# Kernel tuning notes

Hardware: AMD Instinct MI355X
Metric: run time of the kernel (lower is better)

## Reference

```python
import jax, jax.numpy as jnp
import numpy as np

EPS = 1e-6  # flax.linen.LayerNorm default

def layer_norm(x, scale, bias):
    mean = jnp.mean(x, axis=-1, keepdims=True)
    var = jnp.mean(jnp.square(x - mean), axis=-1, keepdims=True)
    return (x - mean) * jax.lax.rsqrt(var + EPS) * scale + bias

def setup_inputs() -> dict:
    key = jax.random.key(0)
    ks = jax.random.split(key, 4)
    B, P, D, H = 2, 2048, 768, 12
    hd = D // H
    x = jax.random.normal(ks[0], (B, P, D), dtype=jnp.float32)
    W_qkv = jax.random.normal(ks[1], (D, 3 * D), dtype=jnp.float32) * (D ** -0.5)
    W_out = jax.random.normal(ks[2], (D, D), dtype=jnp.float32) * (D ** -0.5)
    b_out = jnp.zeros((D,), dtype=jnp.float32)
    return {
        "x": x,
        "W_qkv": W_qkv,
        "q_scale": jnp.ones((hd,), jnp.float32),
        "q_bias": jnp.zeros((hd,), jnp.float32),
        "k_scale": jnp.ones((hd,), jnp.float32),
        "k_bias": jnp.zeros((hd,), jnp.float32),
        "o_scale": jnp.ones((D,), jnp.float32),
        "o_bias": jnp.zeros((D,), jnp.float32),
        "W_out": W_out,
        "b_out": b_out,
    }

def reference(x, W_qkv, q_scale, q_bias, k_scale, k_bias, o_scale, o_bias, W_out, b_out):
    B, P, D = x.shape
    H = 12
    hd = D // H
    scale = hd ** -0.5
    # fused QKV projection, no bias
    qkv = (x @ W_qkv).reshape(B, P, 3, H, hd).transpose(2, 0, 3, 1, 4)  # [3,B,H,P,hd]
    q, k, v = qkv[0], qkv[1], qkv[2]
    # per-head QK LayerNorm over head_dim
    q = layer_norm(q, q_scale, q_bias) * scale
    k = layer_norm(k, k_scale, k_bias)
    attn = jnp.einsum("bhqd,bhkd->bhqk", q, k)
    attn = jax.nn.softmax(attn, axis=-1)
    out = jnp.einsum("bhqk,bhkd->bhqd", attn, v)  # [B,H,P,hd]
    out = jnp.swapaxes(out, 1, 2).reshape(B, P, D)
    out = layer_norm(out, o_scale, o_bias)
    return out @ W_out + b_out
```

## Files before the change

### kernel.cpp

```cpp
#include <hip/hip_runtime.h>
#include <hip/hip_bf16.h>

#define B_  2
#define P_  2048
#define D_  768
#define H_  12
#define HD_ 64
#define M_  (B_ * P_)
#define N1_ (3 * D_)

typedef __attribute__((ext_vector_type(8))) short short8;
typedef __attribute__((ext_vector_type(4))) float f32x4;
typedef __attribute__((ext_vector_type(16))) float f32x16;
typedef __attribute__((ext_vector_type(4))) unsigned u32x4;
typedef unsigned short ushort;

__device__ __forceinline__ ushort f2bf(float f) {
    unsigned u = __float_as_uint(f);
    u += 0x7fffu + ((u >> 16) & 1u);
    return (ushort)(u >> 16);
}

__device__ __forceinline__ unsigned cvtpk(float a, float b) {
    unsigned r;
    asm("v_cvt_pk_bf16_f32 %0, %1, %2" : "=v"(r) : "v"(a), "v"(b));
    return r;
}

__device__ __forceinline__ float bf2f(ushort u) {
    return __uint_as_float((unsigned)u << 16);
}

__device__ __forceinline__ int swap23(int s) {
    return (s & ~12) | ((s & 4) << 1) | ((s & 8) >> 1);
}

#define QSC_ (0.125f * 1.44269504088896340736f)

__global__ __launch_bounds__(512) void gemm_qkv_mfma(
        const float* __restrict__ x, const float* __restrict__ w,
        const float* __restrict__ qs, const float* __restrict__ qb,
        const float* __restrict__ ks, const float* __restrict__ kb,
        ushort* __restrict__ qkv) {
    __shared__ __align__(16) ushort As[2][128][40];
    __shared__ __align__(16) ushort Bs[2][128][40];

    const int tid  = threadIdx.x;
    const int lane = tid & 63;
    const int wv   = tid >> 6;
    const int quad = lane >> 4;
    const int col  = lane & 15;
    const int wr   = (wv >> 1) * 32;
    const int wc   = (wv & 1) * 64;
    const int rowBase = blockIdx.y * 128;
    const int colBase = blockIdx.x * 128;

    const int am0 = tid >> 3, ac4 = tid & 7;
    const int nB  = tid & 127, kq = tid >> 7;

    float4 apre[2];
    float  bpre[8];
    auto load_tile = [&](int kt) {
        const int k0 = kt * 32;
        apre[0] = *(const float4*)(x + (size_t)(rowBase + am0) * D_ + k0 + ac4 * 4);
        apre[1] = *(const float4*)(x + (size_t)(rowBase + am0 + 64) * D_ + k0 + ac4 * 4);
#pragma unroll
        for (int j = 0; j < 8; j++)
            bpre[j] = w[(size_t)(k0 + kq * 8 + j) * N1_ + colBase + nB];
    };
    auto stage = [&](int buf) {
        uint2 a0 = {cvtpk(apre[0].x, apre[0].y), cvtpk(apre[0].z, apre[0].w)};
        uint2 a1 = {cvtpk(apre[1].x, apre[1].y), cvtpk(apre[1].z, apre[1].w)};
        *(uint2*)&As[buf][am0][ac4 * 4]      = a0;
        *(uint2*)&As[buf][am0 + 64][ac4 * 4] = a1;
        u32x4 bb;
#pragma unroll
        for (int j = 0; j < 4; j++) bb[j] = cvtpk(bpre[2 * j], bpre[2 * j + 1]);
        *(u32x4*)&Bs[buf][nB][kq * 8] = bb;
    };

    f32x4 acc[2][4];
#pragma unroll
    for (int i = 0; i < 2; i++)
#pragma unroll
        for (int j = 0; j < 4; j++) acc[i][j] = (f32x4){0.f, 0.f, 0.f, 0.f};

    load_tile(0);
    stage(0);
    __syncthreads();

    const int NT = D_ / 32;
    int cur = 0;
    for (int kt = 0; kt < NT; kt++) {
        const bool more = (kt + 1 < NT);
        if (more) load_tile(kt + 1);

        short8 af[2], bf[4];
#pragma unroll
        for (int mt = 0; mt < 2; mt++) af[mt] = *(const short8*)&As[cur][wr + mt * 16 + col][quad * 8];
#pragma unroll
        for (int nt = 0; nt < 4; nt++) bf[nt] = *(const short8*)&Bs[cur][wc + nt * 16 + col][quad * 8];
#pragma unroll
        for (int mt = 0; mt < 2; mt++)
#pragma unroll
            for (int nt = 0; nt < 4; nt++)
                acc[mt][nt] = __builtin_amdgcn_mfma_f32_16x16x32_bf16(af[mt], bf[nt], acc[mt][nt], 0, 0, 0);

        if (more) {
            stage(cur ^ 1);
            __syncthreads();
            cur ^= 1;
        }
    }

    const int comp = colBase / D_;
    const int rem  = colBase + wc - comp * D_;
    const int h    = rem >> 6;
    float sc4[4] = {0, 0, 0, 0}, bi4[4] = {0, 0, 0, 0};
    if (comp == 0) {
#pragma unroll
        for (int nt = 0; nt < 4; nt++) { sc4[nt] = qs[nt * 16 + col]; bi4[nt] = qb[nt * 16 + col]; }
    } else if (comp == 1) {
#pragma unroll
        for (int nt = 0; nt < 4; nt++) { sc4[nt] = ks[nt * 16 + col]; bi4[nt] = kb[nt * 16 + col]; }
    }

#pragma unroll
    for (int mt = 0; mt < 2; mt++) {
#pragma unroll
        for (int r = 0; r < 4; r++) {
            int m  = rowBase + wr + mt * 16 + quad * 4 + r;
            int bb = m >> 11;
            int p  = m & 2047;
            float v0 = acc[mt][0][r], v1 = acc[mt][1][r], v2 = acc[mt][2][r], v3 = acc[mt][3][r];
            if (comp < 2) {
                float s = v0 + v1 + v2 + v3;
#pragma unroll
                for (int off = 1; off < 16; off <<= 1) s += __shfl_xor(s, off, 64);
                float mean = s * (1.0f / 64.0f);
                float d0 = v0 - mean, d1 = v1 - mean, d2 = v2 - mean, d3 = v3 - mean;
                float sq = d0 * d0 + d1 * d1 + d2 * d2 + d3 * d3;
#pragma unroll
                for (int off = 1; off < 16; off <<= 1) sq += __shfl_xor(sq, off, 64);
                float inv = rsqrtf(sq * (1.0f / 64.0f) + 1e-6f);
                v0 = d0 * inv * sc4[0] + bi4[0];
                v1 = d1 * inv * sc4[1] + bi4[1];
                v2 = d2 * inv * sc4[2] + bi4[2];
                v3 = d3 * inv * sc4[3] + bi4[3];
                if (comp == 0) { v0 *= QSC_; v1 *= QSC_; v2 *= QSC_; v3 *= QSC_; }
            }
            size_t base = ((((size_t)comp * B_ + bb) * H_ + h) * P_ + p) * HD_;
            qkv[base +  0 + col] = f2bf(v0);
            qkv[base + 16 + col] = f2bf(v1);
            qkv[base + 32 + col] = f2bf(v2);
            qkv[base + 48 + col] = f2bf(v3);
        }
    }
}

__global__ __launch_bounds__(256) void attn_split(const ushort* __restrict__ qkv,
                                                  ushort* __restrict__ o0, ushort* __restrict__ o1,
                                                  ushort* __restrict__ o2, ushort* __restrict__ o3,
                                                  float* __restrict__ l0, float* __restrict__ l1,
                                                  float* __restrict__ l2, float* __restrict__ l3) {
    const int p0  = blockIdx.x * 128;
    const int bh  = blockIdx.y;
    const int s   = blockIdx.z;
    const int nsp = gridDim.z;
    const int b   = bh / H_, h = bh % H_;
    ushort* opart = (s == 0) ? o0 : (s == 1) ? o1 : (s == 2) ? o2 : o3;
    float*  lpart = (s == 0) ? l0 : (s == 1) ? l1 : (s == 2) ? l2 : l3;
    const int tid  = threadIdx.x;
    const int lane = tid & 63;
    const int wv   = tid >> 6;
    const int half = lane >> 5;
    const int n32  = lane & 31;

    __shared__ __align__(16) ushort KVs[2][2][64][72];

    const size_t hs  = (size_t)P_ * HD_;
    const int    kv0 = s * (P_ / nsp);
    const ushort* qg = qkv + ((size_t)(0 * B_ + b) * H_ + h) * hs + (size_t)(p0 + wv * 32) * HD_;
    const ushort* kg = qkv + ((size_t)(1 * B_ + b) * H_ + h) * hs + (size_t)kv0 * HD_;
    const ushort* vg = qkv + ((size_t)(2 * B_ + b) * H_ + h) * hs + (size_t)kv0 * HD_;

    short8 aq[4];
#pragma unroll
    for (int ks2 = 0; ks2 < 4; ks2++)
        aq[ks2] = *(const short8*)(qg + (size_t)n32 * HD_ + ks2 * 16 + half * 8);

    float lsum = 0.f;
    f32x16 oaccT[2];
#pragma unroll
    for (int nt = 0; nt < 2; nt++)
#pragma unroll
        for (int r = 0; r < 16; r++) oaccT[nt][r] = 0.f;

    const int kr = tid >> 3, kc8 = tid & 7;
    const int krs = swap23(kr);
    const int vd = tid & 63,  vkh = tid >> 6;

    uint4  kpre[2];
    ushort vpre[16];
    auto load_tile = [&](int kt) {
        const ushort* kg_t = kg + (size_t)kt * 64 * HD_;
        const ushort* vg_t = vg + (size_t)kt * 64 * HD_;
        kpre[0] = *(const uint4*)(kg_t + (size_t)kr * HD_ + kc8 * 8);
        kpre[1] = *(const uint4*)(kg_t + (size_t)(kr + 32) * HD_ + kc8 * 8);
#pragma unroll
        for (int j = 0; j < 16; j++)
            vpre[j] = vg_t[(size_t)(vkh * 16 + j) * HD_ + vd];
    };
    auto stage = [&](int buf) {
        *(uint4*)&KVs[buf][0][krs][kc8 * 8]      = kpre[0];
        *(uint4*)&KVs[buf][0][krs + 32][kc8 * 8] = kpre[1];
        *(short8*)&KVs[buf][1][vd][vkh * 16]     = *(short8*)&vpre[0];
        *(short8*)&KVs[buf][1][vd][vkh * 16 + 8] = *(short8*)&vpre[8];
    };

    load_tile(0);
    stage(0);
    __syncthreads();

    const int NT = (P_ / 64) / nsp;
    int cur = 0;
    for (int kt = 0; kt < NT; kt++) {
        const bool more = (kt + 1 < NT);
        if (more) load_tile(kt + 1);

        ushort (*Ks)[72] = KVs[cur][0];
        ushort (*Vs)[72] = KVs[cur][1];

#pragma unroll
        for (int nt = 0; nt < 2; nt++) {
            f32x16 sc;
#pragma unroll
            for (int r = 0; r < 16; r++) sc[r] = 0.f;
#pragma unroll
            for (int ks2 = 0; ks2 < 4; ks2++) {
                short8 kb2 = *(const short8*)&Ks[nt * 32 + n32][ks2 * 16 + half * 8];
                sc = __builtin_amdgcn_mfma_f32_32x32x16_bf16(kb2, aq[ks2], sc, 0, 0, 0);
            }
            float p[16];
#pragma unroll
            for (int r = 0; r < 16; r++) {
                p[r] = __builtin_amdgcn_exp2f(sc[r]);
                lsum += p[r];
            }
            unsigned w[8];
#pragma unroll
            for (int i = 0; i < 8; i++) w[i] = cvtpk(p[2 * i], p[2 * i + 1]);
#pragma unroll
            for (int kp2 = 0; kp2 < 2; kp2++) {
                u32x4 t = {w[kp2 * 4 + 0], w[kp2 * 4 + 1], w[kp2 * 4 + 2], w[kp2 * 4 + 3]};
                short8 pb = __builtin_bit_cast(short8, t);
                const int kstep = nt * 2 + kp2;
#pragma unroll
                for (int ntd = 0; ntd < 2; ntd++) {
                    short8 av = *(const short8*)&Vs[ntd * 32 + n32][kstep * 16 + half * 8];
                    oaccT[ntd] = __builtin_amdgcn_mfma_f32_32x32x16_bf16(av, pb, oaccT[ntd], 0, 0, 0);
                }
            }
        }

        if (more) {
            stage(cur ^ 1);
            __syncthreads();
            cur ^= 1;
        }
    }

    lsum += __shfl_xor(lsum, 32, 64);
    if (lane < 32)
        lpart[(size_t)bh * P_ + p0 + wv * 32 + lane] = lsum;

    float* scr = (float*)&KVs[0][0][0][0] + wv * 1152;
#pragma unroll
    for (int ntd = 0; ntd < 2; ntd++) {
#pragma unroll
        for (int r = 0; r < 16; r++)
            scr[n32 * 36 + (r & 3) + 8 * (r >> 2) + 4 * half] = oaccT[ntd][r];
#pragma unroll
        for (int i = 0; i < 4; i++) {
            int ql = i * 8 + (lane >> 3);
            int c4 = lane & 7;
            float4 v = *(const float4*)&scr[ql * 36 + c4 * 4];
            uint2 pk = {cvtpk(v.x, v.y), cvtpk(v.z, v.w)};
            *(uint2*)(opart + ((size_t)bh * P_ + p0 + wv * 32 + ql) * HD_ + ntd * 32 + c4 * 4) = pk;
        }
    }
}

__global__ __launch_bounds__(256) void ln_o(const ushort* __restrict__ o0,
                                            const ushort* __restrict__ o1,
                                            const ushort* __restrict__ o2,
                                            const ushort* __restrict__ o3,
                                            const float* __restrict__ l0,
                                            const float* __restrict__ l1,
                                            const float* __restrict__ l2,
                                            const float* __restrict__ l3,
                                            const int ns,
                                            ushort* __restrict__ lnb,
                                            const float* __restrict__ osc,
                                            const float* __restrict__ ob) {
    __shared__ float red[4];
    __shared__ float red2[4];
    const int row = blockIdx.x;
    const int b   = row >> 11;
    const int p   = row & (P_ - 1);
    const int tid = threadIdx.x;

    auto src = [&](int d) {
        int h = d >> 6;
        size_t lr  = (size_t)(b * H_ + h) * P_ + p;
        size_t idx = lr * HD_ + (d & 63);
        float num = bf2f(o0[idx]) + bf2f(o1[idx]);
        float den = l0[lr] + l1[lr];
        if (ns == 4) { num += bf2f(o2[idx]) + bf2f(o3[idx]); den += l2[lr] + l3[lr]; }
        return num / den;
    };
    float v0 = src(tid);
    float v1 = src(tid + 256);
    float v2 = src(tid + 512);
    float s = v0 + v1 + v2;
#pragma unroll
    for (int o = 32; o > 0; o >>= 1) s += __shfl_xor(s, o, 64);
    if ((tid & 63) == 0) red[tid >> 6] = s;
    __syncthreads();
    float mean = (red[0] + red[1] + red[2] + red[3]) * (1.0f / 768.0f);
    float d0 = v0 - mean, d1 = v1 - mean, d2 = v2 - mean;
    float sq = d0 * d0 + d1 * d1 + d2 * d2;
#pragma unroll
    for (int o = 32; o > 0; o >>= 1) sq += __shfl_xor(sq, o, 64);
    if ((tid & 63) == 0) red2[tid >> 6] = sq;
    __syncthreads();
    float var = (red2[0] + red2[1] + red2[2] + red2[3]) * (1.0f / 768.0f);
    float inv = rsqrtf(var + 1e-6f);
    const size_t base = (size_t)row * D_;
    lnb[base + tid]       = f2bf(d0 * inv * osc[tid]       + ob[tid]);
    lnb[base + tid + 256] = f2bf(d1 * inv * osc[tid + 256] + ob[tid + 256]);
    lnb[base + tid + 512] = f2bf(d2 * inv * osc[tid + 512] + ob[tid + 512]);
}

__global__ __launch_bounds__(256) void gemm_out_mfma(
        const ushort* __restrict__ a, const float* __restrict__ w,
        const float* __restrict__ bias, float* __restrict__ out) {
    __shared__ __align__(16) ushort As[2][64][40];
    __shared__ __align__(16) ushort Bs[2][64][40];

    const int tid  = threadIdx.x;
    const int lane = tid & 63;
    const int wv   = tid >> 6;
    const int quad = lane >> 4;
    const int col  = lane & 15;
    const int wr   = (wv >> 1) * 32;
    const int wc   = (wv & 1) * 32;
    const int rowBase = blockIdx.y * 64;
    const int colBase = blockIdx.x * 64;

    const int am  = tid >> 2, ac8 = tid & 3;
    const int nB  = tid & 63, kq = tid >> 6;

    uint4 apre;
    float bpre[8];
    auto load_tile = [&](int kt) {
        const int k0 = kt * 32;
        apre = *(const uint4*)(a + (size_t)(rowBase + am) * D_ + k0 + ac8 * 8);
#pragma unroll
        for (int j = 0; j < 8; j++)
            bpre[j] = w[(size_t)(k0 + kq * 8 + j) * D_ + colBase + nB];
    };
    auto stage = [&](int buf) {
        *(uint4*)&As[buf][am][ac8 * 8] = apre;
        u32x4 bb;
#pragma unroll
        for (int j = 0; j < 4; j++) bb[j] = cvtpk(bpre[2 * j], bpre[2 * j + 1]);
        *(u32x4*)&Bs[buf][nB][kq * 8] = bb;
    };

    f32x4 acc[2][2];
#pragma unroll
    for (int i = 0; i < 2; i++)
#pragma unroll
        for (int j = 0; j < 2; j++) acc[i][j] = (f32x4){0.f, 0.f, 0.f, 0.f};

    load_tile(0);
    stage(0);
    __syncthreads();

    const int NT = D_ / 32;
    int cur = 0;
    for (int kt = 0; kt < NT; kt++) {
        const bool more = (kt + 1 < NT);
        if (more) load_tile(kt + 1);

        short8 af[2], bf[2];
#pragma unroll
        for (int mt = 0; mt < 2; mt++) af[mt] = *(const short8*)&As[cur][wr + mt * 16 + col][quad * 8];
#pragma unroll
        for (int nt = 0; nt < 2; nt++) bf[nt] = *(const short8*)&Bs[cur][wc + nt * 16 + col][quad * 8];
#pragma unroll
        for (int mt = 0; mt < 2; mt++)
#pragma unroll
            for (int nt = 0; nt < 2; nt++)
                acc[mt][nt] = __builtin_amdgcn_mfma_f32_16x16x32_bf16(af[mt], bf[nt], acc[mt][nt], 0, 0, 0);

        if (more) {
            stage(cur ^ 1);
            __syncthreads();
            cur ^= 1;
        }
    }

    float b2[2];
#pragma unroll
    for (int nt = 0; nt < 2; nt++) b2[nt] = bias[colBase + wc + nt * 16 + col];
#pragma unroll
    for (int mt = 0; mt < 2; mt++) {
#pragma unroll
        for (int r = 0; r < 4; r++) {
            int m = rowBase + wr + mt * 16 + quad * 4 + r;
            float* dst = out + (size_t)m * D_ + colBase + wc;
#pragma unroll
            for (int nt = 0; nt < 2; nt++)
                dst[nt * 16 + col] = acc[mt][nt][r] + b2[nt];
        }
    }
}

extern "C" void kernel_launch(void* const* d_in, const int* in_sizes, int n_in,
                              void* d_out, int out_size, void* d_ws, size_t ws_size,
                              hipStream_t stream) {
    const float* x    = (const float*)d_in[0];
    const float* Wqkv = (const float*)d_in[1];
    const float* qs   = (const float*)d_in[2];
    const float* qb   = (const float*)d_in[3];
    const float* ks   = (const float*)d_in[4];
    const float* kb   = (const float*)d_in[5];
    const float* osc  = (const float*)d_in[6];
    const float* ob   = (const float*)d_in[7];
    const float* Wout = (const float*)d_in[8];
    const float* bout = (const float*)d_in[9];
    float* out = (float*)d_out;

    ushort* qkv = (ushort*)d_ws;
    const size_t qkvE = (size_t)3 * B_ * H_ * P_ * HD_;
    const size_t oE   = (size_t)B_ * H_ * P_ * HD_;
    const size_t lE   = (size_t)B_ * H_ * P_;
    ushort* obase = qkv + qkvE;
    const size_t need4 = (qkvE + 3 * oE) * sizeof(ushort) + 4 * lE * sizeof(float);
    const int nsp = (ws_size >= need4) ? 4 : 2;
    ushort* op[4];
    float* lbase;
    if (nsp == 4) {
        op[0] = obase; op[1] = obase + oE; op[2] = obase + 2 * oE; op[3] = (ushort*)out;
        lbase = (float*)(obase + 3 * oE);
    } else {
        op[0] = obase; op[1] = (ushort*)out; op[2] = obase; op[3] = obase;
        lbase = (float*)(obase + oE);
    }
    float* lp[4] = {lbase, lbase + lE, lbase + 2 * lE, lbase + 3 * lE};
    ushort* ln_buf = qkv;

    gemm_qkv_mfma<<<dim3(N1_ / 128, M_ / 128), 512, 0, stream>>>(x, Wqkv, qs, qb, ks, kb, qkv);
    attn_split<<<dim3(P_ / 128, B_ * H_, nsp), 256, 0, stream>>>(
        qkv, op[0], op[1], op[2], op[3], lp[0], lp[1], lp[2], lp[3]);
    ln_o<<<dim3(M_), 256, 0, stream>>>(
        op[0], op[1], op[2], op[3], lp[0], lp[1], lp[2], lp[3], nsp, ln_buf, osc, ob);
    gemm_out_mfma<<<dim3(D_ / 64, M_ / 64), 256, 0, stream>>>(ln_buf, Wout, bout, out);
}
```

Baseline: 207.6 us.

## Load GEMM A operands straight into registers, deepen K-tile, remap blocks per XCD

Both projection GEMMs stop staging the A operand in shared memory. Each wave loads its own rows from global memory directly in MFMA fragment layout, and only the weight tile goes through LDS. The K step doubles to 64 and the tiles change: 128x64 with 256 threads for QKV, 64x64 for the output GEMM. A 1D grid with an XCD-aware swizzle groups row tiles per XCD for L2 locality. The aim is less LDS traffic and fewer barriers. The cost is uncoalesced, redundant A reads from global memory, since each wave re-reads the full A rows for its column tile.

```diff
diff --git a/kernel.cpp b/kernel.cpp
--- a/kernel.cpp
+++ b/kernel.cpp
@@ -37,46 +37,58 @@
 
 #define QSC_ (0.125f * 1.44269504088896340736f)
 
-__global__ __launch_bounds__(512) void gemm_qkv_mfma(
+__global__ __launch_bounds__(256) void gemm_qkv_mfma(
         const float* __restrict__ x, const float* __restrict__ w,
         const float* __restrict__ qs, const float* __restrict__ qb,
         const float* __restrict__ ks, const float* __restrict__ kb,
         ushort* __restrict__ qkv) {
-    __shared__ __align__(16) ushort As[2][128][40];
-    __shared__ __align__(16) ushort Bs[2][128][40];
+    __shared__ __align__(16) ushort Bs[2][64][72];
+
+    const int L   = blockIdx.x;
+    const int xcd = L & 7;
+    const int idx = L >> 3;
+    const int by  = xcd + 8 * (idx / 36);
+    const int bx  = idx % 36;
+    const int rowBase = by * 128;
+    const int colBase = bx * 64;
 
     const int tid  = threadIdx.x;
     const int lane = tid & 63;
     const int wv   = tid >> 6;
     const int quad = lane >> 4;
     const int col  = lane & 15;
-    const int wr   = (wv >> 1) * 32;
-    const int wc   = (wv & 1) * 64;
-    const int rowBase = blockIdx.y * 128;
-    const int colBase = blockIdx.x * 128;
-
-    const int am0 = tid >> 3, ac4 = tid & 7;
-    const int nB  = tid & 127, kq = tid >> 7;
-
-    float4 apre[2];
-    float  bpre[8];
-    auto load_tile = [&](int kt) {
-        const int k0 = kt * 32;
-        apre[0] = *(const float4*)(x + (size_t)(rowBase + am0) * D_ + k0 + ac4 * 4);
-        apre[1] = *(const float4*)(x + (size_t)(rowBase + am0 + 64) * D_ + k0 + ac4 * 4);
-#pragma unroll
-        for (int j = 0; j < 8; j++)
-            bpre[j] = w[(size_t)(k0 + kq * 8 + j) * N1_ + colBase + nB];
-    };
-    auto stage = [&](int buf) {
-        uint2 a0 = {cvtpk(apre[0].x, apre[0].y), cvtpk(apre[0].z, apre[0].w)};
-        uint2 a1 = {cvtpk(apre[1].x, apre[1].y), cvtpk(apre[1].z, apre[1].w)};
-        *(uint2*)&As[buf][am0][ac4 * 4]      = a0;
-        *(uint2*)&As[buf][am0 + 64][ac4 * 4] = a1;
-        u32x4 bb;
-#pragma unroll
-        for (int j = 0; j < 4; j++) bb[j] = cvtpk(bpre[2 * j], bpre[2 * j + 1]);
-        *(u32x4*)&Bs[buf][nB][kq * 8] = bb;
+
+    const int nB = tid & 63, kg = tid >> 6;
+
+    float bpre[16];
+    auto load_b = [&](int kt) {
+        const int k0 = kt * 64;
+#pragma unroll
+        for (int j = 0; j < 16; j++)
+            bpre[j] = w[(size_t)(k0 + kg * 16 + j) * N1_ + colBase + nB];
+    };
+    auto stage_b = [&](int buf) {
+        u32x4 b0, b1;
+#pragma unroll
+        for (int j = 0; j < 4; j++) b0[j] = cvtpk(bpre[2 * j], bpre[2 * j + 1]);
+#pragma unroll
+        for (int j = 0; j < 4; j++) b1[j] = cvtpk(bpre[8 + 2 * j], bpre[8 + 2 * j + 1]);
+        *(u32x4*)&Bs[buf][nB][kg * 16]     = b0;
+        *(u32x4*)&Bs[buf][nB][kg * 16 + 8] = b1;
+    };
+
+    const float* arow0 = x + (size_t)(rowBase + wv * 32 + col) * D_ + quad * 8;
+    const float* arow1 = arow0 + (size_t)16 * D_;
+    float4 apre[2][2][2];
+    auto load_a = [&](int kt) {
+        const int k0 = kt * 64;
+#pragma unroll
+        for (int k32 = 0; k32 < 2; k32++) {
+            apre[0][k32][0] = *(const float4*)(arow0 + k0 + k32 * 32);
+            apre[0][k32][1] = *(const float4*)(arow0 + k0 + k32 * 32 + 4);
+            apre[1][k32][0] = *(const float4*)(arow1 + k0 + k32 * 32);
+            apre[1][k32][1] = *(const float4*)(arow1 + k0 + k32 * 32 + 4);
+        }
     };
 
     f32x4 acc[2][4];
@@ -85,36 +97,53 @@
 #pragma unroll
         for (int j = 0; j < 4; j++) acc[i][j] = (f32x4){0.f, 0.f, 0.f, 0.f};
 
-    load_tile(0);
-    stage(0);
+    load_a(0);
+    load_b(0);
+    stage_b(0);
     __syncthreads();
 
-    const int NT = D_ / 32;
+    const int NT = D_ / 64;
     int cur = 0;
     for (int kt = 0; kt < NT; kt++) {
         const bool more = (kt + 1 < NT);
-        if (more) load_tile(kt + 1);
-
-        short8 af[2], bf[4];
-#pragma unroll
-        for (int mt = 0; mt < 2; mt++) af[mt] = *(const short8*)&As[cur][wr + mt * 16 + col][quad * 8];
-#pragma unroll
-        for (int nt = 0; nt < 4; nt++) bf[nt] = *(const short8*)&Bs[cur][wc + nt * 16 + col][quad * 8];
+
+        short8 af[2][2];
 #pragma unroll
         for (int mt = 0; mt < 2; mt++)
 #pragma unroll
+            for (int k32 = 0; k32 < 2; k32++) {
+                u32x4 t;
+                t[0] = cvtpk(apre[mt][k32][0].x, apre[mt][k32][0].y);
+                t[1] = cvtpk(apre[mt][k32][0].z, apre[mt][k32][0].w);
+                t[2] = cvtpk(apre[mt][k32][1].x, apre[mt][k32][1].y);
+                t[3] = cvtpk(apre[mt][k32][1].z, apre[mt][k32][1].w);
+                af[mt][k32] = __builtin_bit_cast(short8, t);
+            }
+
+        if (more) { load_a(kt + 1); load_b(kt + 1); }
+
+#pragma unroll
+        for (int k32 = 0; k32 < 2; k32++) {
+            short8 bf[4];
+#pragma unroll
             for (int nt = 0; nt < 4; nt++)
-                acc[mt][nt] = __builtin_amdgcn_mfma_f32_16x16x32_bf16(af[mt], bf[nt], acc[mt][nt], 0, 0, 0);
+                bf[nt] = *(const short8*)&Bs[cur][nt * 16 + col][k32 * 32 + quad * 8];
+#pragma unroll
+            for (int mt = 0; mt < 2; mt++)
+#pragma unroll
+                for (int nt = 0; nt < 4; nt++)
+                    acc[mt][nt] = __builtin_amdgcn_mfma_f32_16x16x32_bf16(af[mt][k32], bf[nt], acc[mt][nt], 0, 0, 0);
+        }
 
         if (more) {
-            stage(cur ^ 1);
+            stage_b(cur ^ 1);
             __syncthreads();
             cur ^= 1;
         }
     }
 
     const int comp = colBase / D_;
-    const int rem  = colBase + wc - comp * D_;
+    const int rem  = colBase - comp * D_;
     const int h    = rem >> 6;
     float sc4[4] = {0, 0, 0, 0}, bi4[4] = {0, 0, 0, 0};
     if (comp == 0) {
@@ -129,7 +158,7 @@
     for (int mt = 0; mt < 2; mt++) {
 #pragma unroll
         for (int r = 0; r < 4; r++) {
-            int m  = rowBase + wr + mt * 16 + quad * 4 + r;
+            int m  = rowBase + wv * 32 + mt * 16 + quad * 4 + r;
             int bb = m >> 11;
             int p  = m & 2047;
             float v0 = acc[mt][0][r], v1 = acc[mt][1][r], v2 = acc[mt][2][r], v3 = acc[mt][3][r];
@@ -345,86 +374,96 @@
 __global__ __launch_bounds__(256) void gemm_out_mfma(
         const ushort* __restrict__ a, const float* __restrict__ w,
         const float* __restrict__ bias, float* __restrict__ out) {
-    __shared__ __align__(16) ushort As[2][64][40];
-    __shared__ __align__(16) ushort Bs[2][64][40];
+    __shared__ __align__(16) ushort Bs[2][64][72];
+
+    const int L   = blockIdx.x;
+    const int xcd = L & 7;
+    const int idx = L >> 3;
+    const int by  = xcd + 8 * (idx / 12);
+    const int bx  = idx % 12;
+    const int rowBase = by * 64;
+    const int colBase = bx * 64;
 
     const int tid  = threadIdx.x;
     const int lane = tid & 63;
     const int wv   = tid >> 6;
     const int quad = lane >> 4;
     const int col  = lane & 15;
-    const int wr   = (wv >> 1) * 32;
-    const int wc   = (wv & 1) * 32;
-    const int rowBase = blockIdx.y * 64;
-    const int colBase = blockIdx.x * 64;
-
-    const int am  = tid >> 2, ac8 = tid & 3;
-    const int nB  = tid & 63, kq = tid >> 6;
-
-    uint4 apre;
-    float bpre[8];
-    auto load_tile = [&](int kt) {
-        const int k0 = kt * 32;
-        apre = *(const uint4*)(a + (size_t)(rowBase + am) * D_ + k0 + ac8 * 8);
-#pragma unroll
-        for (int j = 0; j < 8; j++)
-            bpre[j] = w[(size_t)(k0 + kq * 8 + j) * D_ + colBase + nB];
-    };
-    auto stage = [&](int buf) {
-        *(uint4*)&As[buf][am][ac8 * 8] = apre;
-        u32x4 bb;
-#pragma unroll
-        for (int j = 0; j < 4; j++) bb[j] = cvtpk(bpre[2 * j], bpre[2 * j + 1]);
-        *(u32x4*)&Bs[buf][nB][kq * 8] = bb;
-    };
-
-    f32x4 acc[2][2];
-#pragma unroll
-    for (int i = 0; i < 2; i++)
-#pragma unroll
-        for (int j = 0; j < 2; j++) acc[i][j] = (f32x4){0.f, 0.f, 0.f, 0.f};
-
-    load_tile(0);
-    stage(0);
+
+    const int nB = tid & 63, kg = tid >> 6;
+
+    float bpre[16];
+    auto load_b = [&](int kt) {
+        const int k0 = kt * 64;
+#pragma unroll
+        for (int j = 0; j < 16; j++)
+            bpre[j] = w[(size_t)(k0 + kg * 16 + j) * D_ + colBase + nB];
+    };
+    auto stage_b = [&](int buf) {
+        u32x4 b0, b1;
+#pragma unroll
+        for (int j = 0; j < 4; j++) b0[j] = cvtpk(bpre[2 * j], bpre[2 * j + 1]);
+#pragma unroll
+        for (int j = 0; j < 4; j++) b1[j] = cvtpk(bpre[8 + 2 * j], bpre[8 + 2 * j + 1]);
+        *(u32x4*)&Bs[buf][nB][kg * 16]     = b0;
+        *(u32x4*)&Bs[buf][nB][kg * 16 + 8] = b1;
+    };
+
+    const ushort* arow = a + (size_t)(rowBase + wv * 16 + col) * D_ + quad * 8;
+    uint4 apre[2];
+    auto load_a = [&](int kt) {
+        apre[0] = *(const uint4*)(arow + kt * 64);
+        apre[1] = *(const uint4*)(arow + kt * 64 + 32);
+    };
+
+    f32x4 acc[4];
+#pragma unroll
+    for (int j = 0; j < 4; j++) acc[j] = (f32x4){0.f, 0.f, 0.f, 0.f};
+
+    load_a(0);
+    load_b(0);
+    stage_b(0);
     __syncthreads();
 
-    const int NT = D_ / 32;
+    const int NT = D_ / 64;
     int cur = 0;
     for (int kt = 0; kt < NT; kt++) {
         const bool more = (kt + 1 < NT);
-        if (more) load_tile(kt + 1);
-
-        short8 af[2], bf[2];
-#pragma unroll
-        for (int mt = 0; mt < 2; mt++) af[mt] = *(const short8*)&As[cur][wr + mt * 16 + col][quad * 8];
-#pragma unroll
-        for (int nt = 0; nt < 2; nt++) bf[nt] = *(const short8*)&Bs[cur][wc + nt * 16 + col][quad * 8];
-#pragma unroll
-        for (int mt = 0; mt < 2; mt++)
-#pragma unroll
-            for (int nt = 0; nt < 2; nt++)
-                acc[mt][nt] = __builtin_amdgcn_mfma_f32_16x16x32_bf16(af[mt], bf[nt], acc[mt][nt], 0, 0, 0);
+
+        short8 af[2];
+        af[0] = __builtin_bit_cast(short8, apre[0]);
+        af[1] = __builtin_bit_cast(short8, apre[1]);
+
+        if (more) { load_a(kt + 1); load_b(kt + 1); }
+
+#pragma unroll
+        for (int k32 = 0; k32 < 2; k32++) {
+            short8 bf[4];
+#pragma unroll
+            for (int nt = 0; nt < 4; nt++)
+                bf[nt] = *(const short8*)&Bs[cur][nt * 16 + col][k32 * 32 + quad * 8];
+#pragma unroll
+            for (int nt = 0; nt < 4; nt++)
+                acc[nt] = __builtin_amdgcn_mfma_f32_16x16x32_bf16(af[k32], bf[nt], acc[nt], 0, 0, 0);
+        }
 
         if (more) {
-            stage(cur ^ 1);
+            stage_b(cur ^ 1);
             __syncthreads();
             cur ^= 1;
         }
     }
 
-    float b2[2];
-#pragma unroll
-    for (int nt = 0; nt < 2; nt++) b2[nt] = bias[colBase + wc + nt * 16 + col];
-#pragma unroll
-    for (int mt = 0; mt < 2; mt++) {
-#pragma unroll
-        for (int r = 0; r < 4; r++) {
-            int m = rowBase + wr + mt * 16 + quad * 4 + r;
-            float* dst = out + (size_t)m * D_ + colBase + wc;
-#pragma unroll
-            for (int nt = 0; nt < 2; nt++)
-                dst[nt * 16 + col] = acc[mt][nt][r] + b2[nt];
-        }
+    float b2[4];
+#pragma unroll
+    for (int nt = 0; nt < 4; nt++) b2[nt] = bias[colBase + nt * 16 + col];
+#pragma unroll
+    for (int r = 0; r < 4; r++) {
+        int m = rowBase + wv * 16 + quad * 4 + r;
+        float* dst = out + (size_t)m * D_ + colBase;
+#pragma unroll
+        for (int nt = 0; nt < 4; nt++)
+            dst[nt * 16 + col] = acc[nt][r] + b2[nt];
     }
 }
 
@@ -462,10 +501,10 @@
     float* lp[4] = {lbase, lbase + lE, lbase + 2 * lE, lbase + 3 * lE};
     ushort* ln_buf = qkv;
 
-    gemm_qkv_mfma<<<dim3(N1_ / 128, M_ / 128), 512, 0, stream>>>(x, Wqkv, qs, qb, ks, kb, qkv);
+    gemm_qkv_mfma<<<dim3((N1_ / 64) * (M_ / 128)), 256, 0, stream>>>(x, Wqkv, qs, qb, ks, kb, qkv);
     attn_split<<<dim3(P_ / 128, B_ * H_, nsp), 256, 0, stream>>>(
         qkv, op[0], op[1], op[2], op[3], lp[0], lp[1], lp[2], lp[3]);
     ln_o<<<dim3(M_), 256, 0, stream>>>(
         op[0], op[1], op[2], op[3], lp[0], lp[1], lp[2], lp[3], nsp, ln_buf, osc, ob);
-    gemm_out_mfma<<<dim3(D_ / 64, M_ / 64), 256, 0, stream>>>(ln_buf, Wout, bout, out);
-}
+    gemm_out_mfma<<<dim3((D_ / 64) * (M_ / 64)), 256, 0, stream>>>(ln_buf, Wout, bout, out);
+}
```

After: 225.6 us. 1.09x slower.

## Precast inputs and weights to bf16 and single-buffer GEMM LDS staging

Applied to the files above, without the earlier changes.

Adds a grid-stride kernel that converts x, W_qkv and W_out to bf16 in workspace on every call. Both GEMMs then load bf16 directly, which halves their global load bytes and removes the in-loop pack conversions. The double-buffered LDS tiles are also replaced with a single buffer guarded by two barriers per k-step. The cost is an extra full pass over the inputs plus a launch, and less overlap between LDS writes and MFMA work. The weight tiles are still fetched as eight strided 2-byte loads per thread.

```diff
diff --git a/kernel.cpp b/kernel.cpp
--- a/kernel.cpp
+++ b/kernel.cpp
@@ -37,13 +37,36 @@
 
 #define QSC_ (0.125f * 1.44269504088896340736f)
 
+__global__ __launch_bounds__(256) void precast(const float* __restrict__ x,
+                                               const float* __restrict__ wqkv,
+                                               const float* __restrict__ wout,
+                                               ushort* __restrict__ xb,
+                                               ushort* __restrict__ wqb,
+                                               ushort* __restrict__ wob) {
+    const int stride = gridDim.x * 256;
+    int tid = blockIdx.x * 256 + threadIdx.x;
+    const int nx = M_ * D_ / 4, nq = D_ * N1_ / 4, no = D_ * D_ / 4;
+    for (int i = tid; i < nx; i += stride) {
+        float4 v = ((const float4*)x)[i];
+        ((uint2*)xb)[i] = {cvtpk(v.x, v.y), cvtpk(v.z, v.w)};
+    }
+    for (int i = tid; i < nq; i += stride) {
+        float4 v = ((const float4*)wqkv)[i];
+        ((uint2*)wqb)[i] = {cvtpk(v.x, v.y), cvtpk(v.z, v.w)};
+    }
+    for (int i = tid; i < no; i += stride) {
+        float4 v = ((const float4*)wout)[i];
+        ((uint2*)wob)[i] = {cvtpk(v.x, v.y), cvtpk(v.z, v.w)};
+    }
+}
+
 __global__ __launch_bounds__(512) void gemm_qkv_mfma(
-        const float* __restrict__ x, const float* __restrict__ w,
+        const ushort* __restrict__ x, const ushort* __restrict__ w,
         const float* __restrict__ qs, const float* __restrict__ qb,
         const float* __restrict__ ks, const float* __restrict__ kb,
         ushort* __restrict__ qkv) {
-    __shared__ __align__(16) ushort As[2][128][40];
-    __shared__ __align__(16) ushort Bs[2][128][40];
+    __shared__ __align__(16) ushort As[128][40];
+    __shared__ __align__(16) ushort Bs[128][40];
 
     const int tid  = threadIdx.x;
     const int lane = tid & 63;
@@ -55,29 +78,18 @@
     const int rowBase = blockIdx.y * 128;
     const int colBase = blockIdx.x * 128;
 
-    const int am0 = tid >> 3, ac4 = tid & 7;
+    const int amr = tid >> 2, ac4 = tid & 3;
     const int nB  = tid & 127, kq = tid >> 7;
 
-    float4 apre[2];
-    float  bpre[8];
+    uint4  apre;
+    ushort bpre[8];
     auto load_tile = [&](int kt) {
         const int k0 = kt * 32;
-        apre[0] = *(const float4*)(x + (size_t)(rowBase + am0) * D_ + k0 + ac4 * 4);
-        apre[1] = *(const float4*)(x + (size_t)(rowBase + am0 + 64) * D_ + k0 + ac4 * 4);
+        apre = *(const uint4*)(x + (size_t)(rowBase + amr) * D_ + k0 + ac4 * 8);
 #pragma unroll
         for (int j = 0; j < 8; j++)
             bpre[j] = w[(size_t)(k0 + kq * 8 + j) * N1_ + colBase + nB];
     };
-    auto stage = [&](int buf) {
-        uint2 a0 = {cvtpk(apre[0].x, apre[0].y), cvtpk(apre[0].z, apre[0].w)};
-        uint2 a1 = {cvtpk(apre[1].x, apre[1].y), cvtpk(apre[1].z, apre[1].w)};
-        *(uint2*)&As[buf][am0][ac4 * 4]      = a0;
-        *(uint2*)&As[buf][am0 + 64][ac4 * 4] = a1;
-        u32x4 bb;
-#pragma unroll
-        for (int j = 0; j < 4; j++) bb[j] = cvtpk(bpre[2 * j], bpre[2 * j + 1]);
-        *(u32x4*)&Bs[buf][nB][kq * 8] = bb;
-    };
 
     f32x4 acc[2][4];
 #pragma unroll
@@ -86,31 +98,24 @@
         for (int j = 0; j < 4; j++) acc[i][j] = (f32x4){0.f, 0.f, 0.f, 0.f};
 
     load_tile(0);
-    stage(0);
-    __syncthreads();
-
     const int NT = D_ / 32;
-    int cur = 0;
     for (int kt = 0; kt < NT; kt++) {
-        const bool more = (kt + 1 < NT);
-        if (more) load_tile(kt + 1);
+        __syncthreads();
+        *(uint4*)&As[amr][ac4 * 8] = apre;
+        *(short8*)&Bs[nB][kq * 8]  = *(short8*)&bpre[0];
+        __syncthreads();
+        if (kt + 1 < NT) load_tile(kt + 1);
 
         short8 af[2], bf[4];
 #pragma unroll
-        for (int mt = 0; mt < 2; mt++) af[mt] = *(const short8*)&As[cur][wr + mt * 16 + col][quad * 8];
-#pragma unroll
-        for (int nt = 0; nt < 4; nt++) bf[nt] = *(const short8*)&Bs[cur][wc + nt * 16 + col][quad * 8];
+        for (int mt = 0; mt < 2; mt++) af[mt] = *(const short8*)&As[wr + mt * 16 + col][quad * 8];
+#pragma unroll
+        for (int nt = 0; nt < 4; nt++) bf[nt] = *(const short8*)&Bs[wc + nt * 16 + col][quad * 8];
 #pragma unroll
         for (int mt = 0; mt < 2; mt++)
 #pragma unroll
             for (int nt = 0; nt < 4; nt++)
                 acc[mt][nt] = __builtin_amdgcn_mfma_f32_16x16x32_bf16(af[mt], bf[nt], acc[mt][nt], 0, 0, 0);
-
-        if (more) {
-            stage(cur ^ 1);
-            __syncthreads();
-            cur ^= 1;
-        }
     }
 
     const int comp = colBase / D_;
@@ -343,10 +348,10 @@
 }
 
 __global__ __launch_bounds__(256) void gemm_out_mfma(
-        const ushort* __restrict__ a, const float* __restrict__ w,
+        const ushort* __restrict__ a, const ushort* __restrict__ w,
         const float* __restrict__ bias, float* __restrict__ out) {
-    __shared__ __align__(16) ushort As[2][64][40];
-    __shared__ __align__(16) ushort Bs[2][64][40];
+    __shared__ __align__(16) ushort As[64][40];
+    __shared__ __align__(16) ushort Bs[64][40];
 
     const int tid  = threadIdx.x;
     const int lane = tid & 63;
@@ -361,8 +366,8 @@
     const int am  = tid >> 2, ac8 = tid & 3;
     const int nB  = tid & 63, kq = tid >> 6;
 
-    uint4 apre;
-    float bpre[8];
+    uint4  apre;
+    ushort bpre[8];
     auto load_tile = [&](int kt) {
         const int k0 = kt * 32;
         apre = *(const uint4*)(a + (size_t)(rowBase + am) * D_ + k0 + ac8 * 8);
@@ -370,13 +375,6 @@
         for (int j = 0; j < 8; j++)
             bpre[j] = w[(size_t)(k0 + kq * 8 + j) * D_ + colBase + nB];
     };
-    auto stage = [&](int buf) {
-        *(uint4*)&As[buf][am][ac8 * 8] = apre;
-        u32x4 bb;
-#pragma unroll
-        for (int j = 0; j < 4; j++) bb[j] = cvtpk(bpre[2 * j], bpre[2 * j + 1]);
-        *(u32x4*)&Bs[buf][nB][kq * 8] = bb;
-    };
 
     f32x4 acc[2][2];
 #pragma unroll
@@ -385,31 +383,24 @@
         for (int j = 0; j < 2; j++) acc[i][j] = (f32x4){0.f, 0.f, 0.f, 0.f};
 
     load_tile(0);
-    stage(0);
-    __syncthreads();
-
     const int NT = D_ / 32;
-    int cur = 0;
     for (int kt = 0; kt < NT; kt++) {
-        const bool more = (kt + 1 < NT);
-        if (more) load_tile(kt + 1);
+        __syncthreads();
+        *(uint4*)&As[am][ac8 * 8] = apre;
+        *(short8*)&Bs[nB][kq * 8] = *(short8*)&bpre[0];
+        __syncthreads();
+        if (kt + 1 < NT) load_tile(kt + 1);
 
         short8 af[2], bf[2];
 #pragma unroll
-        for (int mt = 0; mt < 2; mt++) af[mt] = *(const short8*)&As[cur][wr + mt * 16 + col][quad * 8];
-#pragma unroll
-        for (int nt = 0; nt < 2; nt++) bf[nt] = *(const short8*)&Bs[cur][wc + nt * 16 + col][quad * 8];
+        for (int mt = 0; mt < 2; mt++) af[mt] = *(const short8*)&As[wr + mt * 16 + col][quad * 8];
+#pragma unroll
+        for (int nt = 0; nt < 2; nt++) bf[nt] = *(const short8*)&Bs[wc + nt * 16 + col][quad * 8];
 #pragma unroll
         for (int mt = 0; mt < 2; mt++)
 #pragma unroll
             for (int nt = 0; nt < 2; nt++)
                 acc[mt][nt] = __builtin_amdgcn_mfma_f32_16x16x32_bf16(af[mt], bf[nt], acc[mt][nt], 0, 0, 0);
-
-        if (more) {
-            stage(cur ^ 1);
-            __syncthreads();
-            cur ^= 1;
-        }
     }
 
     float b2[2];
@@ -444,11 +435,12 @@
     float* out = (float*)d_out;
 
     ushort* qkv = (ushort*)d_ws;
-    const size_t qkvE = (size_t)3 * B_ * H_ * P_ * HD_;
-    const size_t oE   = (size_t)B_ * H_ * P_ * HD_;
-    const size_t lE   = (size_t)B_ * H_ * P_;
+    const size_t qkvE  = (size_t)3 * B_ * H_ * P_ * HD_;
+    const size_t oE    = (size_t)B_ * H_ * P_ * HD_;
+    const size_t lE    = (size_t)B_ * H_ * P_;
+    const size_t castE = (size_t)M_ * D_ + (size_t)D_ * N1_ + (size_t)D_ * D_;
     ushort* obase = qkv + qkvE;
-    const size_t need4 = (qkvE + 3 * oE) * sizeof(ushort) + 4 * lE * sizeof(float);
+    const size_t need4 = (qkvE + 3 * oE + castE) * sizeof(ushort) + 4 * lE * sizeof(float);
     const int nsp = (ws_size >= need4) ? 4 : 2;
     ushort* op[4];
     float* lbase;
@@ -460,12 +452,16 @@
         lbase = (float*)(obase + oE);
     }
     float* lp[4] = {lbase, lbase + lE, lbase + 2 * lE, lbase + 3 * lE};
+    ushort* xb  = (ushort*)(lp[0] + 4 * lE);
+    ushort* wqb = xb + (size_t)M_ * D_;
+    ushort* wob = wqb + (size_t)D_ * N1_;
     ushort* ln_buf = qkv;
 
-    gemm_qkv_mfma<<<dim3(N1_ / 128, M_ / 128), 512, 0, stream>>>(x, Wqkv, qs, qb, ks, kb, qkv);
+    precast<<<dim3(1024), 256, 0, stream>>>(x, Wqkv, Wout, xb, wqb, wob);
+    gemm_qkv_mfma<<<dim3(N1_ / 128, M_ / 128), 512, 0, stream>>>(xb, wqb, qs, qb, ks, kb, qkv);
     attn_split<<<dim3(P_ / 128, B_ * H_, nsp), 256, 0, stream>>>(
         qkv, op[0], op[1], op[2], op[3], lp[0], lp[1], lp[2], lp[3]);
     ln_o<<<dim3(M_), 256, 0, stream>>>(
         op[0], op[1], op[2], op[3], lp[0], lp[1], lp[2], lp[3], nsp, ln_buf, osc, ob);
-    gemm_out_mfma<<<dim3(D_ / 64, M_ / 64), 256, 0, stream>>>(ln_buf, Wout, bout, out);
-}
+    gemm_out_mfma<<<dim3(D_ / 64, M_ / 64), 256, 0, stream>>>(ln_buf, wob, bout, out);
+}
```

Result: no change. 207.0 us (-0.3%).
